# Optimization experiments

Measured on AMD Instinct MI355X. Metric: run time of the kernel, lower is better.

Reference implementation:

```python
import jax, jax.numpy as jnp
import numpy as np

VOXEL_SIZE = 0.04  # metres per voxel (init_kwargs voxel_size)


def setup_inputs() -> dict:
    key = jax.random.key(0)
    k_feat, k_depth, k_zero, k_t = jax.random.split(key, 4)
    B, C, H, W = 4, 32, 120, 160
    X, Y, Z = 128, 128, 64

    features = jax.random.normal(k_feat, (B, C, H, W), dtype=jnp.float32)

    depths = jax.random.uniform(k_depth, (B, H, W), minval=0.5, maxval=5.0)
    zero_mask = jax.random.uniform(k_zero, (B, H, W)) < 0.05
    depths = jnp.where(zero_mask, 0.0, depths).astype(jnp.float32)

    # realistic post-stride intrinsics (f=200 px, principal point at centre)
    K = jnp.array([[200.0, 0.0, 80.0],
                   [0.0, 200.0, 60.0],
                   [0.0, 0.0, 1.0]], dtype=jnp.float32)
    # extrinsics: identity rotation, small per-frame translation
    t = jax.random.uniform(k_t, (B, 3), minval=-0.5, maxval=0.5)
    Rt = jnp.concatenate([jnp.tile(jnp.eye(3, dtype=jnp.float32)[None], (B, 1, 1)),
                          t[:, :, None]], axis=2)              # (B,3,4)
    projection = jnp.einsum('ij,bjk->bik', K, Rt)              # (B,3,4)

    origin = jnp.tile(jnp.array([-3.2, -3.2, 0.0], dtype=jnp.float32)[None], (B, 1))

    return {"origin": origin, "projection": projection, "features": features,
            "depths": depths, "X": X, "Y": Y, "Z": Z}


def reference(origin, projection, features, depths, X, Y, Z):
    B, C, H, W = features.shape
    HW = H * W
    XYZ = X * Y * Z

    # pixel grid: torch.meshgrid(arange(H), arange(W)) -> v over rows, u over cols
    v, u = jnp.meshgrid(jnp.arange(H, dtype=features.dtype),
                        jnp.arange(W, dtype=features.dtype), indexing='ij')
    d = depths                                                  # (B,H,W)
    uvd = jnp.stack([u[None] * d, v[None] * d, d, jnp.ones_like(d)],
                    axis=1).reshape(B, 4, HW)                   # (B,4,HW)

    # homogenise projection and invert per batch
    bottom = jnp.tile(jnp.array([[[0.0, 0.0, 0.0, 1.0]]], dtype=projection.dtype),
                      (B, 1, 1))
    proj4 = jnp.concatenate([projection, bottom], axis=1)       # (B,4,4)
    proj_inv = jnp.linalg.inv(proj4)
    world = jnp.einsum('bij,bjp->bip', proj_inv, uvd)[:, :3]    # (B,3,HW)

    voxel_id = jnp.round((world - origin[:, :, None]) / VOXEL_SIZE).astype(jnp.int32)

    depth_mask = (depths.reshape(B, HW) > 0)
    in_x = (voxel_id[:, 0] >= 0) & (voxel_id[:, 0] < X)
    in_y = (voxel_id[:, 1] >= 0) & (voxel_id[:, 1] < Y)
    in_z = (voxel_id[:, 2] >= 0) & (voxel_id[:, 2] < Z)
    mask = depth_mask & in_x & in_y & in_z                      # (B,HW)

    # flat voxel index; invalid pixels routed out-of-bounds and dropped by scatter
    lin = voxel_id[:, 0] * (Y * Z) + voxel_id[:, 1] * Z + voxel_id[:, 2]
    lin = jnp.where(mask, lin, XYZ)                             # (B,HW)

    feat_flat = features.reshape(B, C, HW)

    def scatter_one(lin_b, feat_b):
        vol = jnp.zeros((C, XYZ), dtype=features.dtype).at[:, lin_b].set(
            feat_b, mode='drop')
        val = jnp.zeros((XYZ,), dtype=features.dtype).at[lin_b].set(
            1.0, mode='drop')
        return vol, val

    volume, valid = jax.vmap(scatter_one)(lin, feat_flat)
    return volume.reshape(B, C, X, Y, Z), valid.reshape(B, 1, X, Y, Z)
```

## Files before the change

kernel.cpp:

```cpp
#include <hip/hip_runtime.h>

#define IMG_W 160
#define VOXEL 0.04f

__device__ __forceinline__ void make_inv(const float* __restrict__ proj, int b,
                                         float inv[12]) {
  const float* P = proj + b * 12;
  const float p00 = P[0], p01 = P[1], p02 = P[2], p03 = P[3];
  const float p11 = P[5], p12 = P[6], p13 = P[7];
  const float p22 = P[10], p23 = P[11];
  const float i00 = __fdiv_rn(1.0f, p00);
  const float i11 = __fdiv_rn(1.0f, p11);
  const float i22 = __fdiv_rn(1.0f, p22);
  const float i01 = __fmul_rn(-i11, __fmul_rn(p01, i00));
  float x0 = __fmul_rn(p02, i00);
  x0 = __fmaf_rn(p12, i01, x0);
  const float x1 = __fmul_rn(p12, i11);
  const float i02 = __fmul_rn(-i22, x0);
  const float i12 = __fmul_rn(-i22, x1);
  float y0 = __fmul_rn(p03, i00);
  y0 = __fmaf_rn(p13, i01, y0);
  float y1 = __fmul_rn(p13, i11);
  y0 = __fmaf_rn(p23, i02, y0);
  y1 = __fmaf_rn(p23, i12, y1);
  const float y2 = __fmul_rn(p23, i22);
  inv[0] = i00;  inv[1] = i01;  inv[2] = i02;   inv[3] = -y0;
  inv[4] = 0.0f; inv[5] = i11;  inv[6] = i12;   inv[7] = -y1;
  inv[8] = 0.0f; inv[9] = 0.0f; inv[10] = i22;  inv[11] = -y2;
}

__device__ __forceinline__ int voxel_lin(const float* __restrict__ origin,
                                         const float* __restrict__ proj,
                                         float d, int b, int p,
                                         int X, int Y, int Z) {
  float inv[12];
  make_inv(proj, b, inv);
  const float u = (float)(p % IMG_W);
  const float v = (float)(p / IMG_W);
  const float uvd0 = __fmul_rn(u, d);
  const float uvd1 = __fmul_rn(v, d);
  const float uvd[4] = { uvd0, uvd1, d, 1.0f };
  float w[3];
#pragma unroll
  for (int r = 0; r < 3; ++r) {
    float acc = 0.0f;
#pragma unroll
    for (int j = 0; j < 4; ++j)
      acc = __fadd_rn(acc, __fmul_rn(inv[r * 4 + j], uvd[j]));
    w[r] = acc;
  }
  const float ox = origin[b * 3 + 0];
  const float oy = origin[b * 3 + 1];
  const float oz = origin[b * 3 + 2];
  const float cx = __fdiv_rn(__fsub_rn(w[0], ox), VOXEL);
  const float cy = __fdiv_rn(__fsub_rn(w[1], oy), VOXEL);
  const float cz = __fdiv_rn(__fsub_rn(w[2], oz), VOXEL);
  const int ix = (int)rintf(cx);
  const int iy = (int)rintf(cy);
  const int iz = (int)rintf(cz);
  if (ix < 0 || ix >= X || iy < 0 || iy >= Y || iz < 0 || iz >= Z) return -1;
  return (ix * Y + iy) * Z + iz;
}

__global__ void k_winner(const float* __restrict__ origin,
                         const float* __restrict__ proj,
                         const float* __restrict__ depths,
                         const int* __restrict__ Xp, const int* __restrict__ Yp,
                         const int* __restrict__ Zp,
                         int* __restrict__ winner, int B, int HW) {
  const int gid = blockIdx.x * blockDim.x + threadIdx.x;
  if (gid >= B * HW) return;
  const int b = gid / HW;
  const int p = gid - b * HW;
  const float d = depths[gid];
  if (!(d > 0.0f)) return;
  const int X = *Xp, Y = *Yp, Z = *Zp;
  const int lin = voxel_lin(origin, proj, d, b, p, X, Y, Z);
  if (lin < 0) return;
  atomicMax(&winner[b * (X * Y * Z) + lin], p + 1);
}

__global__ void k_scatter(const float* __restrict__ origin,
                          const float* __restrict__ proj,
                          const float* __restrict__ depths,
                          const float* __restrict__ feats,
                          const int* __restrict__ Xp, const int* __restrict__ Yp,
                          const int* __restrict__ Zp,
                          float* __restrict__ volume, float* __restrict__ validf,
                          int B, int HW, int C) {
  const int gid = blockIdx.x * blockDim.x + threadIdx.x;
  if (gid >= B * HW) return;
  const int b = gid / HW;
  const int p = gid - b * HW;
  const float d = depths[gid];
  if (!(d > 0.0f)) return;
  const int X = *Xp, Y = *Yp, Z = *Zp;
  const int lin = voxel_lin(origin, proj, d, b, p, X, Y, Z);
  if (lin < 0) return;
  const long long XYZ = (long long)X * Y * Z;
  const long long vox = (long long)b * XYZ + lin;
  const int w = ((const int*)validf)[vox];
  if (w != p + 1) return;
#pragma unroll 4
  for (int c = 0; c < C; ++c)
    volume[((long long)(b * C + c)) * XYZ + lin] =
        feats[(long long)(b * C + c) * HW + p];
  validf[vox] = 1.0f;
}

extern "C" void kernel_launch(void* const* d_in, const int* in_sizes, int n_in,
                              void* d_out, int out_size, void* d_ws, size_t ws_size,
                              hipStream_t stream) {
  const float* origin = (const float*)d_in[0];
  const float* proj   = (const float*)d_in[1];
  const float* feats  = (const float*)d_in[2];
  const float* depths = (const float*)d_in[3];
  const int*   Xp     = (const int*)d_in[4];
  const int*   Yp     = (const int*)d_in[5];
  const int*   Zp     = (const int*)d_in[6];

  const int B  = in_sizes[0] / 3;
  const int HW = in_sizes[3] / B;
  const int C  = in_sizes[2] / (B * HW);
  const long long XYZ = (long long)out_size / (B * (C + 1));

  float* volume = (float*)d_out;
  float* validf = volume + (long long)B * C * XYZ;

  hipMemsetAsync(d_out, 0, (size_t)out_size * sizeof(float), stream);

  const int total = B * HW;
  const int block = 256;
  const int grid  = (total + block - 1) / block;

  k_winner<<<grid, block, 0, stream>>>(origin, proj, depths, Xp, Yp, Zp,
                                       (int*)validf, B, HW);
  k_scatter<<<grid, block, 0, stream>>>(origin, proj, depths, feats, Xp, Yp, Zp,
                                        volume, validf, B, HW, C);
}
```

Before: 599.7 us.

## Replace full-output memset and scatter with a voxel-parallel resolve that writes every output

Drops the memset of the whole output volume. A small kernel now zeroes only the winner buffer, and a new voxel-parallel resolve kernel writes every output element exactly once with float4 stores, gathering features for occupied voxels and writing zeros elsewhere. This removes the double write of the large output, once by memset and once by scatter, at the cost of gathered feature reads per occupied voxel. It assumes XYZ is a power of two and divisible by 4. If the workspace is too small it falls back to the valid buffer, which looks unsafe because the resolve kernel reads winners and writes valid at the same addresses.

New measurement: 670.7 us. +11.8%, slower.

```diff
diff --git a/kernel.cpp b/kernel.cpp
--- a/kernel.cpp
+++ b/kernel.cpp
@@ -37,9 +37,7 @@
   make_inv(proj, b, inv);
   const float u = (float)(p % IMG_W);
   const float v = (float)(p / IMG_W);
-  const float uvd0 = __fmul_rn(u, d);
-  const float uvd1 = __fmul_rn(v, d);
-  const float uvd[4] = { uvd0, uvd1, d, 1.0f };
+  const float uvd[4] = { __fmul_rn(u, d), __fmul_rn(v, d), d, 1.0f };
   float w[3];
 #pragma unroll
   for (int r = 0; r < 3; ++r) {
@@ -49,17 +47,20 @@
       acc = __fadd_rn(acc, __fmul_rn(inv[r * 4 + j], uvd[j]));
     w[r] = acc;
   }
-  const float ox = origin[b * 3 + 0];
-  const float oy = origin[b * 3 + 1];
-  const float oz = origin[b * 3 + 2];
-  const float cx = __fdiv_rn(__fsub_rn(w[0], ox), VOXEL);
-  const float cy = __fdiv_rn(__fsub_rn(w[1], oy), VOXEL);
-  const float cz = __fdiv_rn(__fsub_rn(w[2], oz), VOXEL);
+  const float cx = __fdiv_rn(__fsub_rn(w[0], origin[b * 3 + 0]), VOXEL);
+  const float cy = __fdiv_rn(__fsub_rn(w[1], origin[b * 3 + 1]), VOXEL);
+  const float cz = __fdiv_rn(__fsub_rn(w[2], origin[b * 3 + 2]), VOXEL);
   const int ix = (int)rintf(cx);
   const int iy = (int)rintf(cy);
   const int iz = (int)rintf(cz);
   if (ix < 0 || ix >= X || iy < 0 || iy >= Y || iz < 0 || iz >= Z) return -1;
   return (ix * Y + iy) * Z + iz;
+}
+
+__global__ void k_zero(int* __restrict__ w, long long n4) {
+  const long long t = (long long)blockIdx.x * blockDim.x + threadIdx.x;
+  if (t >= n4) return;
+  *(int4*)&w[t << 2] = make_int4(0, 0, 0, 0);
 }
 
 __global__ void k_winner(const float* __restrict__ origin,
@@ -77,35 +78,51 @@
   const int X = *Xp, Y = *Yp, Z = *Zp;
   const int lin = voxel_lin(origin, proj, d, b, p, X, Y, Z);
   if (lin < 0) return;
-  atomicMax(&winner[b * (X * Y * Z) + lin], p + 1);
+  atomicMax(&winner[((long long)b << 20 >= 0 ? (long long)b * (X * Y * Z) : 0) + lin], p + 1);
 }
 
-__global__ void k_scatter(const float* __restrict__ origin,
-                          const float* __restrict__ proj,
-                          const float* __restrict__ depths,
-                          const float* __restrict__ feats,
-                          const int* __restrict__ Xp, const int* __restrict__ Yp,
-                          const int* __restrict__ Zp,
-                          float* __restrict__ volume, float* __restrict__ validf,
-                          int B, int HW, int C) {
-  const int gid = blockIdx.x * blockDim.x + threadIdx.x;
-  if (gid >= B * HW) return;
-  const int b = gid / HW;
-  const int p = gid - b * HW;
-  const float d = depths[gid];
-  if (!(d > 0.0f)) return;
-  const int X = *Xp, Y = *Yp, Z = *Zp;
-  const int lin = voxel_lin(origin, proj, d, b, p, X, Y, Z);
-  if (lin < 0) return;
-  const long long XYZ = (long long)X * Y * Z;
-  const long long vox = (long long)b * XYZ + lin;
-  const int w = ((const int*)validf)[vox];
-  if (w != p + 1) return;
-#pragma unroll 4
-  for (int c = 0; c < C; ++c)
-    volume[((long long)(b * C + c)) * XYZ + lin] =
-        feats[(long long)(b * C + c) * HW + p];
-  validf[vox] = 1.0f;
+__global__ void k_resolve(const float* __restrict__ feats,
+                          const int* __restrict__ winner,
+                          float* __restrict__ volume,
+                          float* __restrict__ validf,
+                          long long nt, int shXYZ, int C, int HW) {
+  const long long t = (long long)blockIdx.x * blockDim.x + threadIdx.x;
+  if (t >= nt) return;
+  const int shQ = shXYZ - 2;
+  const int b = (int)(t >> shQ);
+  const long long lin = (t & (((long long)1 << shQ) - 1)) << 2;
+  const long long pbase = (long long)b << shXYZ;
+  const int4 w4 = *(const int4*)&winner[pbase + lin];
+  const bool ok0 = (w4.x > 0) & (w4.x <= HW);
+  const bool ok1 = (w4.y > 0) & (w4.y <= HW);
+  const bool ok2 = (w4.z > 0) & (w4.z <= HW);
+  const bool ok3 = (w4.w > 0) & (w4.w <= HW);
+
+  float4 vm;
+  vm.x = ok0 ? 1.0f : 0.0f;
+  vm.y = ok1 ? 1.0f : 0.0f;
+  vm.z = ok2 ? 1.0f : 0.0f;
+  vm.w = ok3 ? 1.0f : 0.0f;
+  *(float4*)&validf[pbase + lin] = vm;
+
+  float* __restrict__ vol = volume + ((long long)(b * C) << shXYZ) + lin;
+  if (!(ok0 | ok1 | ok2 | ok3)) {
+    const float4 z4 = make_float4(0.0f, 0.0f, 0.0f, 0.0f);
+    for (int c = 0; c < C; ++c)
+      *(float4*)&vol[(long long)c << shXYZ] = z4;
+    return;
+  }
+  const int i0 = w4.x - 1, i1 = w4.y - 1, i2 = w4.z - 1, i3 = w4.w - 1;
+  const float* __restrict__ fb = feats + (long long)(b * C) * HW;
+  for (int c = 0; c < C; ++c) {
+    const float* __restrict__ fc = fb + (long long)c * HW;
+    float4 o = make_float4(0.0f, 0.0f, 0.0f, 0.0f);
+    if (ok0) o.x = fc[i0];
+    if (ok1) o.y = fc[i1];
+    if (ok2) o.z = fc[i2];
+    if (ok3) o.w = fc[i3];
+    *(float4*)&vol[(long long)c << shXYZ] = o;
+  }
 }
 
 extern "C" void kernel_launch(void* const* d_in, const int* in_sizes, int n_in,
@@ -127,14 +144,25 @@
   float* volume = (float*)d_out;
   float* validf = volume + (long long)B * C * XYZ;
 
-  hipMemsetAsync(d_out, 0, (size_t)out_size * sizeof(float), stream);
+  int shXYZ = 0; while (((long long)1 << shXYZ) < XYZ) ++shXYZ;
 
-  const int total = B * HW;
+  const size_t winner_bytes = (size_t)(B * XYZ) * sizeof(int);
+  int* winner = (ws_size >= winner_bytes) ? (int*)d_ws : (int*)validf;
+
   const int block = 256;
-  const int grid  = (total + block - 1) / block;
 
-  k_winner<<<grid, block, 0, stream>>>(origin, proj, depths, Xp, Yp, Zp,
-                                       (int*)validf, B, HW);
-  k_scatter<<<grid, block, 0, stream>>>(origin, proj, depths, feats, Xp, Yp, Zp,
-                                        volume, validf, B, HW, C);
+  {
+    const long long n4 = ((long long)B * XYZ) >> 2;
+    k_zero<<<(int)((n4 + block - 1) / block), block, 0, stream>>>(winner, n4);
+  }
+  {
+    const int total = B * HW;
+    k_winner<<<(total + block - 1) / block, block, 0, stream>>>(
+        origin, proj, depths, Xp, Yp, Zp, winner, B, HW);
+  }
+  {
+    const long long nt = ((long long)B * XYZ) >> 2;
+    k_resolve<<<(int)((nt + block - 1) / block), block, 0, stream>>>(
+        feats, winner, volume, validf, nt, shXYZ, C, HW);
+  }
 }
```
